# Kernel optimization log

Hardware: AMD Instinct MI355X
Metric: run time of the kernel (lower is better)

The kernel has to match this reference:

```python
import jax, jax.numpy as jnp
import numpy as np

H = 128
NH = 8  # num attention heads


def _ln(x, g, b, eps=1e-5):
    m = x.mean(-1, keepdims=True)
    v = ((x - m) ** 2).mean(-1, keepdims=True)
    return (x - m) / jnp.sqrt(v + eps) * g + b


def _mha(q_in, kv_in, Wqkv, bqkv, Wo, bo):
    # torch nn.MultiheadAttention with packed in_proj, batch=1, eval (no dropout)
    h = q_in.shape[-1]
    hd = h // NH
    Wq, Wk, Wv = Wqkv[:h], Wqkv[h:2 * h], Wqkv[2 * h:]
    bq, bk, bv = bqkv[:h], bqkv[h:2 * h], bqkv[2 * h:]
    q = (q_in @ Wq.T + bq).reshape(-1, NH, hd).transpose(1, 0, 2)   # [nh, Nq, hd]
    k = (kv_in @ Wk.T + bk).reshape(-1, NH, hd).transpose(1, 0, 2)  # [nh, Nk, hd]
    v = (kv_in @ Wv.T + bv).reshape(-1, NH, hd).transpose(1, 0, 2)
    scores = jnp.einsum('hqd,hkd->hqk', q, k) / jnp.sqrt(jnp.asarray(hd, q.dtype))
    attn = jax.nn.softmax(scores, axis=-1)
    out = jnp.einsum('hqk,hkd->hqd', attn, v)                       # [nh, Nq, hd]
    out = out.transpose(1, 0, 2).reshape(-1, h)
    return out @ Wo.T + bo


def setup_inputs() -> dict:
    key = jax.random.key(0)
    ks = jax.random.split(key, 32)
    s = 0.05
    d = {
        'ligand_features': jax.random.normal(ks[0], (512, 128), jnp.float32),
        'pocket_features': jax.random.normal(ks[1], (1024, 128), jnp.float32),
        'ligand_coords': jax.random.uniform(ks[2], (512, 3), jnp.float32) * 20.0,
        'pocket_coords': jax.random.uniform(ks[3], (1024, 3), jnp.float32) * 20.0,
        # projections
        'Wl': jax.random.normal(ks[4], (H, 128), jnp.float32) * s,
        'bl': jnp.zeros((H,), jnp.float32),
        'Wp': jax.random.normal(ks[5], (H, 128), jnp.float32) * s,
        'bp': jnp.zeros((H,), jnp.float32),
        # distance encoder: 1 -> h/4 -> h/2 -> h
        'Wd1': jax.random.normal(ks[6], (H // 4, 1), jnp.float32) * s,
        'bd1': jnp.zeros((H // 4,), jnp.float32),
        'Wd2': jax.random.normal(ks[7], (H // 2, H // 4), jnp.float32) * s,
        'bd2': jnp.zeros((H // 2,), jnp.float32),
        'Wd3': jax.random.normal(ks[8], (H, H // 2), jnp.float32) * s,
        'bd3': jnp.zeros((H,), jnp.float32),
        # gates
        'Wgl': jax.random.normal(ks[9], (H, 2 * H), jnp.float32) * s,
        'bgl': jnp.zeros((H,), jnp.float32),
        'Wgp': jax.random.normal(ks[10], (H, 2 * H), jnp.float32) * s,
        'bgp': jnp.zeros((H,), jnp.float32),
        # shared cross-attention (packed qkv like torch)
        'Wqkv': jax.random.normal(ks[11], (3 * H, H), jnp.float32) * s,
        'bqkv': jnp.zeros((3 * H,), jnp.float32),
        'Wo': jax.random.normal(ks[12], (H, H), jnp.float32) * s,
        'bo': jnp.zeros((H,), jnp.float32),
        # layer norms
        'g_l': jnp.ones((H,), jnp.float32),
        'be_l': jnp.zeros((H,), jnp.float32),
        'g_p': jnp.ones((H,), jnp.float32),
        'be_p': jnp.zeros((H,), jnp.float32),
    }
    return d


def reference(ligand_features, pocket_features, ligand_coords, pocket_coords,
              Wl, bl, Wp, bp, Wd1, bd1, Wd2, bd2, Wd3, bd3,
              Wgl, bgl, Wgp, bgp, Wqkv, bqkv, Wo, bo,
              g_l, be_l, g_p, be_p):
    lig = ligand_features @ Wl.T + bl   # [Nl, H]
    poc = pocket_features @ Wp.T + bp   # [Np, H]

    # pairwise distances [Nl, Np]
    diff = ligand_coords[:, None, :] - pocket_coords[None, :, :]
    dist = jnp.sqrt(jnp.sum(diff * diff, axis=-1))

    # distance encoder MLP applied elementwise -> [Nl, Np, H]
    e = jax.nn.relu(dist[..., None] @ Wd1.T + bd1)
    e = jax.nn.relu(e @ Wd2.T + bd2)
    enc = e @ Wd3.T + bd3
    m = enc.mean(axis=-1)               # [Nl, Np]

    # ligand enhancement: softmax over pocket axis
    sw_l = jax.nn.softmax(-m, axis=-1)          # [Nl, Np]
    agg_l = sw_l @ poc                          # [Nl, H]
    gate_l = jax.nn.sigmoid(jnp.concatenate([lig, agg_l], axis=-1) @ Wgl.T + bgl)
    lig_enh = gate_l * lig + (1.0 - gate_l) * agg_l

    # pocket enhancement: transposed encoding, softmax over ligand axis
    sw_p = jax.nn.softmax(-m.T, axis=-1)        # [Np, Nl]
    agg_p = sw_p @ lig                          # [Np, H]
    gate_p = jax.nn.sigmoid(jnp.concatenate([poc, agg_p], axis=-1) @ Wgp.T + bgp)
    poc_enh = gate_p * poc + (1.0 - gate_p) * agg_p

    lig_att = _mha(lig_enh, poc_enh, Wqkv, bqkv, Wo, bo)
    poc_att = _mha(poc_enh, lig_enh, Wqkv, bqkv, Wo, bo)

    lig_fused = _ln(lig_enh + lig_att, g_l, be_l)
    poc_fused = _ln(poc_enh + poc_att, g_p, be_p)
    return (lig_fused, poc_fused)
```

## Files before the change

kernel.cpp:

```cpp
#include <hip/hip_runtime.h>
#include <math.h>

#define NL 512
#define NP 1024
#define HDIM 128

#define TAB_N 8192
#define DMAX 34.65f

#define M_OFF    128
#define WLT_OFF  (M_OFF)
#define WPT_OFF  (M_OFF + 16384)
#define WQT_OFF  (M_OFF + 32768)
#define WOT_OFF  (M_OFF + 81920)
#define WGLT_OFF (M_OFF + 98304)
#define WGPT_OFF (M_OFF + 131072)
#define LIG_OFF  (M_OFF + NL*NP)
#define POC_OFF  (LIG_OFF + NL*HDIM)
#define LENH_OFF (POC_OFF + NP*HDIM)
#define PENH_OFF (LENH_OFF + NL*HDIM)
#define QKVL_OFF (PENH_OFF + NP*HDIM)
#define QKVP_OFF (QKVL_OFF + NL*384)
#define PARTL_OFF (QKVP_OFF + NP*384)
#define PARTP_OFF (PARTL_OFF + 512*8*8*18)
#define TAB_OFF  QKVL_OFF

__device__ __forceinline__ float dot4f(float4 a, float4 b){
  return fmaf(a.x,b.x, fmaf(a.y,b.y, fmaf(a.z,b.z, a.w*b.w)));
}

__device__ __forceinline__ void tpose(const float* __restrict__ src, float* __restrict__ dst,
                                      int O, int K, int blk0, int t){
  int e0 = blk0*1024 + t*4;
  #pragma unroll
  for (int i = 0; i < 4; i++){
    int e = e0 + i;
    int o = e / K, k = e - o*K;
    dst[(size_t)k*O + o] = src[(size_t)o*K + k];
  }
}
__global__ __launch_bounds__(256) void transpose_all(const float* __restrict__ Wl, const float* __restrict__ Wp,
                                                     const float* __restrict__ Wqkv, const float* __restrict__ Wo,
                                                     const float* __restrict__ Wgl, const float* __restrict__ Wgp,
                                                     float* __restrict__ ws){
  int b = blockIdx.x, t = threadIdx.x;
  if      (b < 16)  tpose(Wl,   ws + WLT_OFF,  128, 128, b,       t);
  else if (b < 32)  tpose(Wp,   ws + WPT_OFF,  128, 128, b - 16,  t);
  else if (b < 80)  tpose(Wqkv, ws + WQT_OFF,  384, 128, b - 32,  t);
  else if (b < 96)  tpose(Wo,   ws + WOT_OFF,  128, 128, b - 80,  t);
  else if (b < 128) tpose(Wgl,  ws + WGLT_OFF, 128, 256, b - 96,  t);
  else              tpose(Wgp,  ws + WGPT_OFF, 128, 256, b - 128, t);
}

__global__ __launch_bounds__(256) void table_kernel(const float* __restrict__ Wd1, const float* __restrict__ bd1,
                                                    const float* __restrict__ Wd2, const float* __restrict__ bd2,
                                                    const float* __restrict__ Wd3, const float* __restrict__ bd3,
                                                    float* __restrict__ tab){
  __shared__ float sWd1[32], sbd1[32], sWd2[2048], sbd2[64], swd3m[64];
  __shared__ float sbd3m;
  int t = threadIdx.x;
  int idx = blockIdx.x * 256 + t;
  if (t < 64){
    float s = 0.f;
    #pragma unroll 8
    for (int i = 0; i < 128; i++) s += Wd3[i*64 + t];
    swd3m[t] = s * (1.f/128.f);
  } else if (t == 64){
    float s = 0.f;
    for (int i = 0; i < 128; i++) s += bd3[i];
    sbd3m = s * (1.f/128.f);
  } else if (t >= 128 && t < 160){ sWd1[t-128] = Wd1[t-128]; sbd1[t-128] = bd1[t-128]; }
  else if (t >= 160 && t < 224){ sbd2[t-160] = bd2[t-160]; }
  for (int k = t; k < 2048; k += 256) sWd2[k] = Wd2[k];
  __syncthreads();

  float d = (float)idx * (DMAX / (float)(TAB_N - 1));

  float4 e1q[8];
  const float4* w1q = (const float4*)sWd1;
  const float4* b1q = (const float4*)sbd1;
  #pragma unroll
  for (int k4 = 0; k4 < 8; k4++){
    float4 w = w1q[k4], b = b1q[k4];
    float4 e;
    e.x = fmaxf(fmaf(d, w.x, b.x), 0.f);
    e.y = fmaxf(fmaf(d, w.y, b.y), 0.f);
    e.z = fmaxf(fmaf(d, w.z, b.z), 0.f);
    e.w = fmaxf(fmaf(d, w.w, b.w), 0.f);
    e1q[k4] = e;
  }
  float mv = sbd3m;
  #pragma unroll 4
  for (int j2 = 0; j2 < 64; j2++){
    const float4* wrow = (const float4*)(sWd2 + j2*32);
    float a0 = 0.f, a1 = 0.f, a2 = 0.f, a3 = 0.f;
    #pragma unroll
    for (int k4 = 0; k4 < 8; k4++){
      float4 w = wrow[k4], e = e1q[k4];
      a0 = fmaf(w.x, e.x, a0);
      a1 = fmaf(w.y, e.y, a1);
      a2 = fmaf(w.z, e.z, a2);
      a3 = fmaf(w.w, e.w, a3);
    }
    float e2v = fmaxf(sbd2[j2] + ((a0+a1)+(a2+a3)), 0.f);
    mv = fmaf(swd3m[j2], e2v, mv);
  }
  tab[idx] = mv;
}

__global__ __launch_bounds__(1024) void proj_kernel(const float* __restrict__ lf, const float* __restrict__ pf,
                                                    const float* __restrict__ WlT, const float* __restrict__ bl,
                                                    const float* __restrict__ WpT, const float* __restrict__ bp,
                                                    float* __restrict__ lig, float* __restrict__ poc){
  int b = blockIdx.x, t = threadIdx.x;
  bool isLig = (b < 64);
  int r0 = isLig ? b*8 : (b - 64)*8;
  const float* in = (isLig ? lf : pf) + (size_t)r0*HDIM;
  const float* WT = isLig ? WlT : WpT;
  const float* bias = isLig ? bl : bp;
  float* out = (isLig ? lig : poc) + (size_t)r0*HDIM;
  __shared__ float sx[8*HDIM];
  sx[t] = in[t];
  __syncthreads();
  int r = t >> 7, col = t & 127;
  const float* xr = sx + r*HDIM;
  float acc = bias[col];
  #pragma unroll 8
  for (int k = 0; k < 128; k++) acc = fmaf(WT[k*128 + col], xr[k], acc);
  out[r*HDIM + col] = acc;
}

__global__ __launch_bounds__(1024) void agg_gate_fused(const float* __restrict__ lc, const float* __restrict__ pc,
                                                       const float* __restrict__ tab,
                                                       const float* __restrict__ lig, const float* __restrict__ poc,
                                                       const float* __restrict__ WglT, const float* __restrict__ bgl,
                                                       const float* __restrict__ WgpT, const float* __restrict__ bgp,
                                                       float* __restrict__ lenh, float* __restrict__ penh){
  int b = blockIdx.x, t = threadIdx.x;
  bool isLig = (b < NL/4);
  int r0 = isLig ? b*4 : (b - NL/4)*4;
  int n = isLig ? NP : NL;
  const float* myFeat = isLig ? lig : poc;
  const float* otherFeat = isLig ? poc : lig;
  const float* myC = isLig ? lc : pc;
  const float* otC = isLig ? pc : lc;

  __shared__ float w[4*NP];
  __shared__ float sx[4*HDIM];
  __shared__ float sa[4*HDIM];
  __shared__ float part[16*512];
  __shared__ float redm[16];
  __shared__ float sgm[4], sinv[4];

  int rr = t >> 8, u = t & 255;
  int lane = t & 63, wv = t >> 6;
  int row = r0 + rr;

  if (t < 512) sx[t] = myFeat[(size_t)r0*HDIM + t];

  float cx = myC[row*3+0], cy = myC[row*3+1], cz = myC[row*3+2];
  const float inv_h = (float)(TAB_N - 1) / DMAX;
  int per = n >> 8;

  float xs[4];
  float lmax = -1e30f;
  for (int k = 0; k < per; k++){
    int j = u + (k << 8);
    float ox = otC[j*3+0], oy = otC[j*3+1], oz = otC[j*3+2];
    float dx = cx-ox, dy = cy-oy, dz = cz-oz;
    float d = sqrtf(fmaf(dx,dx, fmaf(dy,dy, dz*dz)));
    float xf = d * inv_h;
    int i0 = (int)xf;
    i0 = (i0 > TAB_N-2) ? (TAB_N-2) : i0;
    float f = xf - (float)i0;
    float v0 = tab[i0], v1 = tab[i0+1];
    xs[k] = -fmaf(f, v1 - v0, v0);
    lmax = fmaxf(lmax, xs[k]);
  }
  float v = lmax;
  #pragma unroll
  for (int off = 32; off; off >>= 1) v = fmaxf(v, __shfl_down(v, off));
  if (lane == 0) redm[wv] = v;
  __syncthreads();
  if (t < 4) sgm[t] = fmaxf(fmaxf(redm[t*4+0], redm[t*4+1]), fmaxf(redm[t*4+2], redm[t*4+3]));
  __syncthreads();
  float gm = sgm[rr];
  float lsum = 0.f;
  for (int k = 0; k < per; k++){
    float e = __expf(xs[k] - gm);
    w[rr*NP + u + (k << 8)] = e;
    lsum += e;
  }
  v = lsum;
  #pragma unroll
  for (int off = 32; off; off >>= 1) v += __shfl_down(v, off);
  if (lane == 0) redm[wv] = v;
  __syncthreads();
  if (t < 4) sinv[t] = 1.0f / ((redm[t*4+0] + redm[t*4+1]) + (redm[t*4+2] + redm[t*4+3]));
  __syncthreads();

  {
    int jg = t >> 6;
    int rp = (t >> 5) & 1;
    int c4 = t & 31;
    int per2 = n >> 4;
    int jb0 = jg * per2;
    int rA = rp*2, rB = rp*2 + 1;
    const float4* of4 = (const float4*)otherFeat;
    const float* wA = w + rA*NP;
    const float* wB = w + rB*NP;
    float4 accA = {0,0,0,0}, accB = {0,0,0,0};
    #pragma unroll 4
    for (int jj = 0; jj < per2; jj++){
      int j = jb0 + jj;
      float4 f = of4[(size_t)j*32 + c4];
      float w0 = wA[j], w1 = wB[j];
      accA.x = fmaf(w0, f.x, accA.x); accA.y = fmaf(w0, f.y, accA.y);
      accA.z = fmaf(w0, f.z, accA.z); accA.w = fmaf(w0, f.w, accA.w);
      accB.x = fmaf(w1, f.x, accB.x); accB.y = fmaf(w1, f.y, accB.y);
      accB.z = fmaf(w1, f.z, accB.z); accB.w = fmaf(w1, f.w, accB.w);
    }
    float4* p4 = (float4*)part;
    p4[jg*128 + rA*32 + c4] = accA;
    p4[jg*128 + rB*32 + c4] = accB;
  }
  __syncthreads();
  {
    float4* p4 = (float4*)part;
    #pragma unroll
    for (int s = 8; s >= 1; s >>= 1){
      if (t < s*128){
        int jg2 = t >> 7, rem = t & 127;
        float4 a = p4[jg2*128 + rem], bb = p4[(jg2+s)*128 + rem];
        a.x += bb.x; a.y += bb.y; a.z += bb.z; a.w += bb.w;
        p4[jg2*128 + rem] = a;
      }
      __syncthreads();
    }
  }
  if (t < 512){
    int r = t >> 7;
    sa[t] = part[t] * sinv[r];
  }
  __syncthreads();

  if (t < 512){
    int r = t >> 7, col = t & 127;
    const float* WT = isLig ? WglT : WgpT;
    const float* bg = isLig ? bgl : bgp;
    const float* xr = sx + r*HDIM;
    const float* ar = sa + r*HDIM;
    float g = bg[col];
    #pragma unroll 8
    for (int k = 0; k < 128; k++) g = fmaf(WT[k*128 + col], xr[k], g);
    #pragma unroll 8
    for (int k = 0; k < 128; k++) g = fmaf(WT[(128+k)*128 + col], ar[k], g);
    g = 1.0f / (1.0f + __expf(-g));
    float xv = xr[col], av = ar[col];
    float* dst = isLig ? (lenh + (size_t)(r0+r)*HDIM) : (penh + (size_t)(r0+r)*HDIM);
    dst[col] = fmaf(g, xv - av, av);
  }
}

__global__ __launch_bounds__(768) void qkv_kernel(const float* __restrict__ lenh, const float* __restrict__ penh,
                                                  const float* __restrict__ WqkvT, const float* __restrict__ bqkv,
                                                  float* __restrict__ qkvl, float* __restrict__ qkvp){
  int b = blockIdx.x, t = threadIdx.x;
  int row0 = b*2;
  bool isLig = (row0 < NL);
  int rloc = isLig ? row0 : row0 - NL;
  const float* in = (isLig ? lenh : penh) + (size_t)rloc*HDIM;
  float* out = (isLig ? qkvl : qkvp) + (size_t)rloc*384;
  __shared__ float sx[2*HDIM];
  if (t < 256) sx[t] = in[t];
  __syncthreads();
  int r = (t >= 384) ? 1 : 0;
  int col = t - r*384;
  const float* xr = sx + r*HDIM;
  float acc = bqkv[col];
  #pragma unroll 8
  for (int k = 0; k < 128; k++) acc = fmaf(WqkvT[k*384 + col], xr[k], acc);
  out[r*384 + col] = acc;
}

__global__ __launch_bounds__(256) void attn_part(const float* __restrict__ qkvl, const float* __restrict__ qkvp,
                                                 float* __restrict__ partL, float* __restrict__ partP){
  int bx = blockIdx.x;
  int t = threadIdx.x;
  const float* qsrc; const float* kvsrc; int qt, slice; bool isLig;
  if (bx < 256){ isLig = true;  qt = bx >> 3; slice = bx & 7; qsrc = qkvl; kvsrc = qkvp; }
  else { int b2 = bx - 256; isLig = false; qt = b2 >> 2; slice = b2 & 3; qsrc = qkvp; kvsrc = qkvl; }
  int g = t >> 7, tt = t & 127;
  int h = tt >> 4, q = tt & 15;
  int j0 = slice*128 + g*64;

  const float4* qp = (const float4*)(qsrc + (size_t)(qt*16+q)*384 + h*16);
  float4 q0 = qp[0], q1 = qp[1], q2 = qp[2], q3 = qp[3];
  float m = -1e30f, l = 0.f;
  float4 O0 = {0,0,0,0}, O1 = {0,0,0,0}, O2 = {0,0,0,0}, O3 = {0,0,0,0};

  __shared__ float sKV[8192];
  float* myKV = sKV + g*4096;

  for (int tile = 0; tile < 4; tile++){
    int jbase = j0 + tile*16;
    __syncthreads();
    #pragma unroll
    for (int n = 0; n < 8; n++){
      int v4 = tt + n*128;
      int jj = v4 >> 6, c4 = v4 & 63;
      ((float4*)myKV)[(size_t)jj*64 + c4] = *(const float4*)(kvsrc + (size_t)(jbase+jj)*384 + 128 + c4*4);
    }
    __syncthreads();
    float s[16];
    #pragma unroll
    for (int jj = 0; jj < 16; jj++){
      const float4* kk = (const float4*)(myKV + jj*256 + h*16);
      s[jj] = (dot4f(q0, kk[0]) + dot4f(q1, kk[1]) + dot4f(q2, kk[2]) + dot4f(q3, kk[3])) * 0.25f;
    }
    float mt = s[0];
    #pragma unroll
    for (int jj = 1; jj < 16; jj++) mt = fmaxf(mt, s[jj]);
    float mn = fmaxf(m, mt);
    float corr = __expf(m - mn);
    l *= corr;
    O0.x*=corr; O0.y*=corr; O0.z*=corr; O0.w*=corr;
    O1.x*=corr; O1.y*=corr; O1.z*=corr; O1.w*=corr;
    O2.x*=corr; O2.y*=corr; O2.z*=corr; O2.w*=corr;
    O3.x*=corr; O3.y*=corr; O3.z*=corr; O3.w*=corr;
    #pragma unroll
    for (int jj = 0; jj < 16; jj++){
      float p = __expf(s[jj] - mn);
      l += p;
      const float4* vv = (const float4*)(myKV + jj*256 + 128 + h*16);
      O0.x = fmaf(p, vv[0].x, O0.x); O0.y = fmaf(p, vv[0].y, O0.y);
      O0.z = fmaf(p, vv[0].z, O0.z); O0.w = fmaf(p, vv[0].w, O0.w);
      O1.x = fmaf(p, vv[1].x, O1.x); O1.y = fmaf(p, vv[1].y, O1.y);
      O1.z = fmaf(p, vv[1].z, O1.z); O1.w = fmaf(p, vv[1].w, O1.w);
      O2.x = fmaf(p, vv[2].x, O2.x); O2.y = fmaf(p, vv[2].y, O2.y);
      O2.z = fmaf(p, vv[2].z, O2.z); O2.w = fmaf(p, vv[2].w, O2.w);
      O3.x = fmaf(p, vv[3].x, O3.x); O3.y = fmaf(p, vv[3].y, O3.y);
      O3.z = fmaf(p, vv[3].z, O3.z); O3.w = fmaf(p, vv[3].w, O3.w);
    }
    m = mn;
  }

  __syncthreads();
  float* smerge = sKV;
  if (g == 1){
    float* b = smerge + tt*19;
    b[0] = m; b[1] = l;
    b[2]=O0.x; b[3]=O0.y; b[4]=O0.z; b[5]=O0.w;
    b[6]=O1.x; b[7]=O1.y; b[8]=O1.z; b[9]=O1.w;
    b[10]=O2.x; b[11]=O2.y; b[12]=O2.z; b[13]=O2.w;
    b[14]=O3.x; b[15]=O3.y; b[16]=O3.z; b[17]=O3.w;
  }
  __syncthreads();
  if (g == 0){
    const float* b = smerge + tt*19;
    float m1 = b[0], l1 = b[1];
    float M = fmaxf(m, m1);
    float e0 = __expf(m - M), e1 = __expf(m1 - M);
    float L = l*e0 + l1*e1;
    float* dst;
    if (isLig) dst = partL + ((size_t)((qt*16+q)*8 + h)*8 + slice)*18;
    else       dst = partP + ((size_t)((qt*16+q)*8 + h)*4 + slice)*18;
    dst[0] = M; dst[1] = L;
    dst[2]  = O0.x*e0 + b[2]*e1;  dst[3]  = O0.y*e0 + b[3]*e1;
    dst[4]  = O0.z*e0 + b[4]*e1;  dst[5]  = O0.w*e0 + b[5]*e1;
    dst[6]  = O1.x*e0 + b[6]*e1;  dst[7]  = O1.y*e0 + b[7]*e1;
    dst[8]  = O1.z*e0 + b[8]*e1;  dst[9]  = O1.w*e0 + b[9]*e1;
    dst[10] = O2.x*e0 + b[10]*e1; dst[11] = O2.y*e0 + b[11]*e1;
    dst[12] = O2.z*e0 + b[12]*e1; dst[13] = O2.w*e0 + b[13]*e1;
    dst[14] = O3.x*e0 + b[14]*e1; dst[15] = O3.y*e0 + b[15]*e1;
    dst[16] = O3.z*e0 + b[16]*e1; dst[17] = O3.w*e0 + b[17]*e1;
  }
}

__global__ __launch_bounds__(1024) void merge_ln(const float* __restrict__ partL, const float* __restrict__ partP,
                                                 const float* __restrict__ lenh, const float* __restrict__ penh,
                                                 const float* __restrict__ WoT, const float* __restrict__ bo,
                                                 const float* __restrict__ g_l, const float* __restrict__ be_l,
                                                 const float* __restrict__ g_p, const float* __restrict__ be_p,
                                                 float* __restrict__ out){
  int b = blockIdx.x, t = threadIdx.x;
  int r0 = b*8;
  int r = t >> 7, c = t & 127;
  int gr = r0 + r;
  int h = c >> 4, cc = c & 15;
  int ns; const float* base;
  if (gr < NL){ ns = 8; base = partL + ((size_t)(gr*8 + h))*8*18; }
  else        { ns = 4; base = partP + ((size_t)((gr-NL)*8 + h))*4*18; }
  float M = -1e30f;
  for (int s = 0; s < ns; s++) M = fmaxf(M, base[s*18]);
  float Lsum = 0.f, Osum = 0.f;
  for (int s = 0; s < ns; s++){
    float e = __expf(base[s*18] - M);
    Lsum = fmaf(e, base[s*18+1], Lsum);
    Osum = fmaf(e, base[s*18+2+cc], Osum);
  }
  __shared__ float sAtt[8*HDIM];
  sAtt[t] = Osum / Lsum;
  __syncthreads();
  float o = bo[c];
  const float* sA = sAtt + r*HDIM;
  #pragma unroll 8
  for (int k = 0; k < 128; k++) o = fmaf(WoT[k*128 + c], sA[k], o);
  const float* enh = (gr < NL) ? (lenh + (size_t)gr*HDIM) : (penh + (size_t)(gr-NL)*HDIM);
  float x = enh[c] + o;
  __shared__ float sred[32];
  int wid = t >> 6;
  float v = x;
  #pragma unroll
  for (int off = 32; off; off >>= 1) v += __shfl_down(v, off);
  if ((t & 63) == 0) sred[wid] = v;
  __syncthreads();
  float mu = (sred[2*r] + sred[2*r+1]) * (1.f/128.f);
  float dx = x - mu;
  v = dx*dx;
  #pragma unroll
  for (int off = 32; off; off >>= 1) v += __shfl_down(v, off);
  if ((t & 63) == 0) sred[16 + wid] = v;
  __syncthreads();
  float var = (sred[16 + 2*r] + sred[16 + 2*r+1]) * (1.f/128.f);
  float y = dx * rsqrtf(var + 1e-5f);
  if (gr < NL) y = fmaf(y, g_l[c], be_l[c]);
  else         y = fmaf(y, g_p[c], be_p[c]);
  out[(size_t)gr*HDIM + c] = y;
}

extern "C" void kernel_launch(void* const* d_in, const int* in_sizes, int n_in,
                              void* d_out, int out_size, void* d_ws, size_t ws_size,
                              hipStream_t stream){
  const float* lf   = (const float*)d_in[0];
  const float* pf   = (const float*)d_in[1];
  const float* lc   = (const float*)d_in[2];
  const float* pc   = (const float*)d_in[3];
  const float* Wl   = (const float*)d_in[4];
  const float* bl   = (const float*)d_in[5];
  const float* Wp   = (const float*)d_in[6];
  const float* bp   = (const float*)d_in[7];
  const float* Wd1  = (const float*)d_in[8];
  const float* bd1  = (const float*)d_in[9];
  const float* Wd2  = (const float*)d_in[10];
  const float* bd2  = (const float*)d_in[11];
  const float* Wd3  = (const float*)d_in[12];
  const float* bd3  = (const float*)d_in[13];
  const float* Wgl  = (const float*)d_in[14];
  const float* bgl  = (const float*)d_in[15];
  const float* Wgp  = (const float*)d_in[16];
  const float* bgp  = (const float*)d_in[17];
  const float* Wqkv = (const float*)d_in[18];
  const float* bqkv = (const float*)d_in[19];
  const float* Wo   = (const float*)d_in[20];
  const float* bo   = (const float*)d_in[21];
  const float* g_l  = (const float*)d_in[22];
  const float* be_l = (const float*)d_in[23];
  const float* g_p  = (const float*)d_in[24];
  const float* be_p = (const float*)d_in[25];

  float* ws  = (float*)d_ws;
  float* out = (float*)d_out;
  float* lig   = ws + LIG_OFF;
  float* poc   = ws + POC_OFF;
  float* lenh  = ws + LENH_OFF;
  float* penh  = ws + PENH_OFF;
  float* qkvl  = ws + QKVL_OFF;
  float* qkvp  = ws + QKVP_OFF;
  float* partL = ws + PARTL_OFF;
  float* partP = ws + PARTP_OFF;
  float* tab   = ws + TAB_OFF;

  transpose_all<<<160, 256, 0, stream>>>(Wl, Wp, Wqkv, Wo, Wgl, Wgp, ws);
  table_kernel<<<TAB_N/256, 256, 0, stream>>>(Wd1, bd1, Wd2, bd2, Wd3, bd3, tab);
  proj_kernel<<<192, 1024, 0, stream>>>(lf, pf, ws + WLT_OFF, bl, ws + WPT_OFF, bp, lig, poc);
  agg_gate_fused<<<NL/4 + NP/4, 1024, 0, stream>>>(lc, pc, tab, lig, poc,
                                                   ws + WGLT_OFF, bgl, ws + WGPT_OFF, bgp, lenh, penh);
  qkv_kernel<<<768, 768, 0, stream>>>(lenh, penh, ws + WQT_OFF, bqkv, qkvl, qkvp);
  attn_part<<<512, 256, 0, stream>>>(qkvl, qkvp, partL, partP);
  merge_ln<<<192, 1024, 0, stream>>>(partL, partP, lenh, penh, ws + WOT_OFF, bo,
                                     g_l, be_l, g_p, be_p, out);
}
```

Measured before the change: 209.4 us.

## Fuse prep kernels, fold QKV projection into gate kernel, restructure attention partials

Merges the weight-transpose and distance-table kernels into a single launch, with the table moved to its own workspace slot so it no longer aliases the QKV buffer. The QKV projection is computed inside the aggregation/gate kernel from the enhanced rows still in shared memory, which removes one launch and one global round trip of the enhanced features. The attention partial kernel now has each thread handle two query rows over 4 key groups of 32 instead of 2 groups of 64, so K/V values loaded from shared memory are reused across queries, followed by a 4-way merge. The fused QKV step runs on only 512 of 1024 threads per block, and the attention change raises register pressure.

```diff
diff --git a/kernel.cpp b/kernel.cpp
--- a/kernel.cpp
+++ b/kernel.cpp
@@ -15,6 +15,7 @@
 #define WOT_OFF  (M_OFF + 81920)
 #define WGLT_OFF (M_OFF + 98304)
 #define WGPT_OFF (M_OFF + 131072)
+#define TAB_OFF  (M_OFF + 163840)
 #define LIG_OFF  (M_OFF + NL*NP)
 #define POC_OFF  (LIG_OFF + NL*HDIM)
 #define LENH_OFF (POC_OFF + NP*HDIM)
@@ -23,7 +24,6 @@
 #define QKVP_OFF (QKVL_OFF + NL*384)
 #define PARTL_OFF (QKVP_OFF + NP*384)
 #define PARTP_OFF (PARTL_OFF + 512*8*8*18)
-#define TAB_OFF  QKVL_OFF
 
 __device__ __forceinline__ float dot4f(float4 a, float4 b){
   return fmaf(a.x,b.x, fmaf(a.y,b.y, fmaf(a.z,b.z, a.w*b.w)));
@@ -39,27 +39,27 @@
     dst[(size_t)k*O + o] = src[(size_t)o*K + k];
   }
 }
-__global__ __launch_bounds__(256) void transpose_all(const float* __restrict__ Wl, const float* __restrict__ Wp,
-                                                     const float* __restrict__ Wqkv, const float* __restrict__ Wo,
-                                                     const float* __restrict__ Wgl, const float* __restrict__ Wgp,
-                                                     float* __restrict__ ws){
+__global__ __launch_bounds__(256) void prep_all(const float* __restrict__ Wl, const float* __restrict__ Wp,
+                                                const float* __restrict__ Wqkv, const float* __restrict__ Wo,
+                                                const float* __restrict__ Wgl, const float* __restrict__ Wgp,
+                                                const float* __restrict__ Wd1, const float* __restrict__ bd1,
+                                                const float* __restrict__ Wd2, const float* __restrict__ bd2,
+                                                const float* __restrict__ Wd3, const float* __restrict__ bd3,
+                                                float* __restrict__ ws){
   int b = blockIdx.x, t = threadIdx.x;
-  if      (b < 16)  tpose(Wl,   ws + WLT_OFF,  128, 128, b,       t);
-  else if (b < 32)  tpose(Wp,   ws + WPT_OFF,  128, 128, b - 16,  t);
-  else if (b < 80)  tpose(Wqkv, ws + WQT_OFF,  384, 128, b - 32,  t);
-  else if (b < 96)  tpose(Wo,   ws + WOT_OFF,  128, 128, b - 80,  t);
-  else if (b < 128) tpose(Wgl,  ws + WGLT_OFF, 128, 256, b - 96,  t);
-  else              tpose(Wgp,  ws + WGPT_OFF, 128, 256, b - 128, t);
-}
-
-__global__ __launch_bounds__(256) void table_kernel(const float* __restrict__ Wd1, const float* __restrict__ bd1,
-                                                    const float* __restrict__ Wd2, const float* __restrict__ bd2,
-                                                    const float* __restrict__ Wd3, const float* __restrict__ bd3,
-                                                    float* __restrict__ tab){
+  if (b < 160){
+    if      (b < 16)  tpose(Wl,   ws + WLT_OFF,  128, 128, b,       t);
+    else if (b < 32)  tpose(Wp,   ws + WPT_OFF,  128, 128, b - 16,  t);
+    else if (b < 80)  tpose(Wqkv, ws + WQT_OFF,  384, 128, b - 32,  t);
+    else if (b < 96)  tpose(Wo,   ws + WOT_OFF,  128, 128, b - 80,  t);
+    else if (b < 128) tpose(Wgl,  ws + WGLT_OFF, 128, 256, b - 96,  t);
+    else              tpose(Wgp,  ws + WGPT_OFF, 128, 256, b - 128, t);
+    return;
+  }
+  float* tab = ws + TAB_OFF;
   __shared__ float sWd1[32], sbd1[32], sWd2[2048], sbd2[64], swd3m[64];
   __shared__ float sbd3m;
-  int t = threadIdx.x;
-  int idx = blockIdx.x * 256 + t;
+  int idx = (b - 160) * 256 + t;
   if (t < 64){
     float s = 0.f;
     #pragma unroll 8
@@ -75,18 +75,17 @@
   __syncthreads();
 
   float d = (float)idx * (DMAX / (float)(TAB_N - 1));
-
   float4 e1q[8];
   const float4* w1q = (const float4*)sWd1;
   const float4* b1q = (const float4*)sbd1;
   #pragma unroll
   for (int k4 = 0; k4 < 8; k4++){
-    float4 w = w1q[k4], b = b1q[k4];
+    float4 w = w1q[k4], bb = b1q[k4];
     float4 e;
-    e.x = fmaxf(fmaf(d, w.x, b.x), 0.f);
-    e.y = fmaxf(fmaf(d, w.y, b.y), 0.f);
-    e.z = fmaxf(fmaf(d, w.z, b.z), 0.f);
-    e.w = fmaxf(fmaf(d, w.w, b.w), 0.f);
+    e.x = fmaxf(fmaf(d, w.x, bb.x), 0.f);
+    e.y = fmaxf(fmaf(d, w.y, bb.y), 0.f);
+    e.z = fmaxf(fmaf(d, w.z, bb.z), 0.f);
+    e.w = fmaxf(fmaf(d, w.w, bb.w), 0.f);
     e1q[k4] = e;
   }
   float mv = sbd3m;
@@ -135,7 +134,9 @@
                                                        const float* __restrict__ lig, const float* __restrict__ poc,
                                                        const float* __restrict__ WglT, const float* __restrict__ bgl,
                                                        const float* __restrict__ WgpT, const float* __restrict__ bgp,
-                                                       float* __restrict__ lenh, float* __restrict__ penh){
+                                                       const float* __restrict__ WqkvT, const float* __restrict__ bqkv,
+                                                       float* __restrict__ lenh, float* __restrict__ penh,
+                                                       float* __restrict__ qkvl, float* __restrict__ qkvp){
   int b = blockIdx.x, t = threadIdx.x;
   bool isLig = (b < NL/4);
   int r0 = isLig ? b*4 : (b - NL/4)*4;
@@ -244,43 +245,45 @@
   }
   __syncthreads();
 
+  float enh_val = 0.f;
+  {
+    if (t < 512){
+      int r = t >> 7, col = t & 127;
+      const float* WT = isLig ? WglT : WgpT;
+      const float* bg = isLig ? bgl : bgp;
+      const float* xr = sx + r*HDIM;
+      const float* ar = sa + r*HDIM;
+      float g = bg[col];
+      #pragma unroll 8
+      for (int k = 0; k < 128; k++) g = fmaf(WT[k*128 + col], xr[k], g);
+      #pragma unroll 8
+      for (int k = 0; k < 128; k++) g = fmaf(WT[(128+k)*128 + col], ar[k], g);
+      g = 1.0f / (1.0f + __expf(-g));
+      float xv = xr[col], av = ar[col];
+      enh_val = fmaf(g, xv - av, av);
+      float* dst = isLig ? (lenh + (size_t)(r0+r)*HDIM) : (penh + (size_t)(r0+r)*HDIM);
+      dst[col] = enh_val;
+    }
+  }
+  __syncthreads();
+  if (t < 512) sa[t] = enh_val;
+  __syncthreads();
+
   if (t < 512){
-    int r = t >> 7, col = t & 127;
-    const float* WT = isLig ? WglT : WgpT;
-    const float* bg = isLig ? bgl : bgp;
-    const float* xr = sx + r*HDIM;
-    const float* ar = sa + r*HDIM;
-    float g = bg[col];
-    #pragma unroll 8
-    for (int k = 0; k < 128; k++) g = fmaf(WT[k*128 + col], xr[k], g);
-    #pragma unroll 8
-    for (int k = 0; k < 128; k++) g = fmaf(WT[(128+k)*128 + col], ar[k], g);
-    g = 1.0f / (1.0f + __expf(-g));
-    float xv = xr[col], av = ar[col];
-    float* dst = isLig ? (lenh + (size_t)(r0+r)*HDIM) : (penh + (size_t)(r0+r)*HDIM);
-    dst[col] = fmaf(g, xv - av, av);
-  }
-}
-
-__global__ __launch_bounds__(768) void qkv_kernel(const float* __restrict__ lenh, const float* __restrict__ penh,
-                                                  const float* __restrict__ WqkvT, const float* __restrict__ bqkv,
-                                                  float* __restrict__ qkvl, float* __restrict__ qkvp){
-  int b = blockIdx.x, t = threadIdx.x;
-  int row0 = b*2;
-  bool isLig = (row0 < NL);
-  int rloc = isLig ? row0 : row0 - NL;
-  const float* in = (isLig ? lenh : penh) + (size_t)rloc*HDIM;
-  float* out = (isLig ? qkvl : qkvp) + (size_t)rloc*384;
-  __shared__ float sx[2*HDIM];
-  if (t < 256) sx[t] = in[t];
-  __syncthreads();
-  int r = (t >= 384) ? 1 : 0;
-  int col = t - r*384;
-  const float* xr = sx + r*HDIM;
-  float acc = bqkv[col];
-  #pragma unroll 8
-  for (int k = 0; k < 128; k++) acc = fmaf(WqkvT[k*384 + col], xr[k], acc);
-  out[r*384 + col] = acc;
+    int r = t >> 7, c0 = t & 127;
+    const float* er = sa + r*HDIM;
+    float acc0 = bqkv[c0], acc1 = bqkv[c0+128], acc2 = bqkv[c0+256];
+    #pragma unroll 4
+    for (int k = 0; k < 128; k++){
+      float xv = er[k];
+      const float* wk = WqkvT + k*384;
+      acc0 = fmaf(wk[c0],       xv, acc0);
+      acc1 = fmaf(wk[c0+128],   xv, acc1);
+      acc2 = fmaf(wk[c0+256],   xv, acc2);
+    }
+    float* qout = (isLig ? qkvl : qkvp) + (size_t)(r0+r)*384;
+    qout[c0] = acc0; qout[c0+128] = acc1; qout[c0+256] = acc2;
+  }
 }
 
 __global__ __launch_bounds__(256) void attn_part(const float* __restrict__ qkvl, const float* __restrict__ qkvp,
@@ -290,90 +293,137 @@
   const float* qsrc; const float* kvsrc; int qt, slice; bool isLig;
   if (bx < 256){ isLig = true;  qt = bx >> 3; slice = bx & 7; qsrc = qkvl; kvsrc = qkvp; }
   else { int b2 = bx - 256; isLig = false; qt = b2 >> 2; slice = b2 & 3; qsrc = qkvp; kvsrc = qkvl; }
-  int g = t >> 7, tt = t & 127;
-  int h = tt >> 4, q = tt & 15;
-  int j0 = slice*128 + g*64;
-
-  const float4* qp = (const float4*)(qsrc + (size_t)(qt*16+q)*384 + h*16);
-  float4 q0 = qp[0], q1 = qp[1], q2 = qp[2], q3 = qp[3];
-  float m = -1e30f, l = 0.f;
-  float4 O0 = {0,0,0,0}, O1 = {0,0,0,0}, O2 = {0,0,0,0}, O3 = {0,0,0,0};
+  int g = t >> 6, tt = t & 63;
+  int h = tt >> 3, qp = tt & 7;
+  int j0 = slice*128 + g*32;
+
+  const float4* qA = (const float4*)(qsrc + (size_t)(qt*16+qp)*384 + h*16);
+  const float4* qB = (const float4*)(qsrc + (size_t)(qt*16+qp+8)*384 + h*16);
+  float4 a0 = qA[0], a1 = qA[1], a2 = qA[2], a3 = qA[3];
+  float4 b0 = qB[0], b1 = qB[1], b2 = qB[2], b3 = qB[3];
+  float mA = -1e30f, lA = 0.f, mB = -1e30f, lB = 0.f;
+  float4 OA0={0,0,0,0}, OA1={0,0,0,0}, OA2={0,0,0,0}, OA3={0,0,0,0};
+  float4 OB0={0,0,0,0}, OB1={0,0,0,0}, OB2={0,0,0,0}, OB3={0,0,0,0};
 
   __shared__ float sKV[8192];
-  float* myKV = sKV + g*4096;
+  float* myKV = sKV + g*2048;
 
   for (int tile = 0; tile < 4; tile++){
-    int jbase = j0 + tile*16;
+    int jbase = j0 + tile*8;
     __syncthreads();
     #pragma unroll
-    for (int n = 0; n < 8; n++){
-      int v4 = tt + n*128;
+    for (int nn = 0; nn < 8; nn++){
+      int v4 = tt + nn*64;
       int jj = v4 >> 6, c4 = v4 & 63;
-      ((float4*)myKV)[(size_t)jj*64 + c4] = *(const float4*)(kvsrc + (size_t)(jbase+jj)*384 + 128 + c4*4);
+      ((float4*)myKV)[jj*64 + c4] = *(const float4*)(kvsrc + (size_t)(jbase+jj)*384 + 128 + c4*4);
     }
     __syncthreads();
-    float s[16];
-    #pragma unroll
-    for (int jj = 0; jj < 16; jj++){
+    float sA[8], sB[8];
+    #pragma unroll
+    for (int jj = 0; jj < 8; jj++){
       const float4* kk = (const float4*)(myKV + jj*256 + h*16);
-      s[jj] = (dot4f(q0, kk[0]) + dot4f(q1, kk[1]) + dot4f(q2, kk[2]) + dot4f(q3, kk[3])) * 0.25f;
-    }
-    float mt = s[0];
-    #pragma unroll
-    for (int jj = 1; jj < 16; jj++) mt = fmaxf(mt, s[jj]);
-    float mn = fmaxf(m, mt);
-    float corr = __expf(m - mn);
-    l *= corr;
-    O0.x*=corr; O0.y*=corr; O0.z*=corr; O0.w*=corr;
-    O1.x*=corr; O1.y*=corr; O1.z*=corr; O1.w*=corr;
-    O2.x*=corr; O2.y*=corr; O2.z*=corr; O2.w*=corr;
-    O3.x*=corr; O3.y*=corr; O3.z*=corr; O3.w*=corr;
-    #pragma unroll
-    for (int jj = 0; jj < 16; jj++){
-      float p = __expf(s[jj] - mn);
-      l += p;
+      float4 k0 = kk[0], k1 = kk[1], k2 = kk[2], k3 = kk[3];
+      sA[jj] = (dot4f(a0,k0) + dot4f(a1,k1) + dot4f(a2,k2) + dot4f(a3,k3)) * 0.25f;
+      sB[jj] = (dot4f(b0,k0) + dot4f(b1,k1) + dot4f(b2,k2) + dot4f(b3,k3)) * 0.25f;
+    }
+    float mtA = sA[0], mtB = sB[0];
+    #pragma unroll
+    for (int jj = 1; jj < 8; jj++){ mtA = fmaxf(mtA, sA[jj]); mtB = fmaxf(mtB, sB[jj]); }
+    float mnA = fmaxf(mA, mtA), mnB = fmaxf(mB, mtB);
+    float cA = __expf(mA - mnA), cB = __expf(mB - mnB);
+    lA *= cA; lB *= cB;
+    OA0.x*=cA; OA0.y*=cA; OA0.z*=cA; OA0.w*=cA;
+    OA1.x*=cA; OA1.y*=cA; OA1.z*=cA; OA1.w*=cA;
+    OA2.x*=cA; OA2.y*=cA; OA2.z*=cA; OA2.w*=cA;
+    OA3.x*=cA; OA3.y*=cA; OA3.z*=cA; OA3.w*=cA;
+    OB0.x*=cB; OB0.y*=cB; OB0.z*=cB; OB0.w*=cB;
+    OB1.x*=cB; OB1.y*=cB; OB1.z*=cB; OB1.w*=cB;
+    OB2.x*=cB; OB2.y*=cB; OB2.z*=cB; OB2.w*=cB;
+    OB3.x*=cB; OB3.y*=cB; OB3.z*=cB; OB3.w*=cB;
+    #pragma unroll
+    for (int jj = 0; jj < 8; jj++){
+      float pA = __expf(sA[jj] - mnA);
+      float pB = __expf(sB[jj] - mnB);
+      lA += pA; lB += pB;
       const float4* vv = (const float4*)(myKV + jj*256 + 128 + h*16);
-      O0.x = fmaf(p, vv[0].x, O0.x); O0.y = fmaf(p, vv[0].y, O0.y);
-      O0.z = fmaf(p, vv[0].z, O0.z); O0.w = fmaf(p, vv[0].w, O0.w);
-      O1.x = fmaf(p, vv[1].x, O1.x); O1.y = fmaf(p, vv[1].y, O1.y);
-      O1.z = fmaf(p, vv[1].z, O1.z); O1.w = fmaf(p, vv[1].w, O1.w);
-      O2.x = fmaf(p, vv[2].x, O2.x); O2.y = fmaf(p, vv[2].y, O2.y);
-      O2.z = fmaf(p, vv[2].z, O2.z); O2.w = fmaf(p, vv[2].w, O2.w);
-      O3.x = fmaf(p, vv[3].x, O3.x); O3.y = fmaf(p, vv[3].y, O3.y);
-      O3.z = fmaf(p, vv[3].z, O3.z); O3.w = fmaf(p, vv[3].w, O3.w);
-    }
-    m = mn;
-  }
-
-  __syncthreads();
-  float* smerge = sKV;
-  if (g == 1){
-    float* b = smerge + tt*19;
-    b[0] = m; b[1] = l;
-    b[2]=O0.x; b[3]=O0.y; b[4]=O0.z; b[5]=O0.w;
-    b[6]=O1.x; b[7]=O1.y; b[8]=O1.z; b[9]=O1.w;
-    b[10]=O2.x; b[11]=O2.y; b[12]=O2.z; b[13]=O2.w;
-    b[14]=O3.x; b[15]=O3.y; b[16]=O3.z; b[17]=O3.w;
+      float4 v0 = vv[0], v1 = vv[1], v2 = vv[2], v3 = vv[3];
+      OA0.x = fmaf(pA, v0.x, OA0.x); OA0.y = fmaf(pA, v0.y, OA0.y);
+      OA0.z = fmaf(pA, v0.z, OA0.z); OA0.w = fmaf(pA, v0.w, OA0.w);
+      OA1.x = fmaf(pA, v1.x, OA1.x); OA1.y = fmaf(pA, v1.y, OA1.y);
+      OA1.z = fmaf(pA, v1.z, OA1.z); OA1.w = fmaf(pA, v1.w, OA1.w);
+      OA2.x = fmaf(pA, v2.x, OA2.x); OA2.y = fmaf(pA, v2.y, OA2.y);
+      OA2.z = fmaf(pA, v2.z, OA2.z); OA2.w = fmaf(pA, v2.w, OA2.w);
+      OA3.x = fmaf(pA, v3.x, OA3.x); OA3.y = fmaf(pA, v3.y, OA3.y);
+      OA3.z = fmaf(pA, v3.z, OA3.z); OA3.w = fmaf(pA, v3.w, OA3.w);
+      OB0.x = fmaf(pB, v0.x, OB0.x); OB0.y = fmaf(pB, v0.y, OB0.y);
+      OB0.z = fmaf(pB, v0.z, OB0.z); OB0.w = fmaf(pB, v0.w, OB0.w);
+      OB1.x = fmaf(pB, v1.x, OB1.x); OB1.y = fmaf(pB, v1.y, OB1.y);
+      OB1.z = fmaf(pB, v1.z, OB1.z); OB1.w = fmaf(pB, v1.w, OB1.w);
+      OB2.x = fmaf(pB, v2.x, OB2.x); OB2.y = fmaf(pB, v2.y, OB2.y);
+      OB2.z = fmaf(pB, v2.z, OB2.z); OB2.w = fmaf(pB, v2.w, OB2.w);
+      OB3.x = fmaf(pB, v3.x, OB3.x); OB3.y = fmaf(pB, v3.y, OB3.y);
+      OB3.z = fmaf(pB, v3.z, OB3.z); OB3.w = fmaf(pB, v3.w, OB3.w);
+    }
+    mA = mnA; mB = mnB;
+  }
+
+  __syncthreads();
+  if (g > 0){
+    float* bA = sKV + (size_t)((g-1)*128 + tt*2)*19;
+    bA[0]=mA; bA[1]=lA;
+    bA[2]=OA0.x; bA[3]=OA0.y; bA[4]=OA0.z; bA[5]=OA0.w;
+    bA[6]=OA1.x; bA[7]=OA1.y; bA[8]=OA1.z; bA[9]=OA1.w;
+    bA[10]=OA2.x; bA[11]=OA2.y; bA[12]=OA2.z; bA[13]=OA2.w;
+    bA[14]=OA3.x; bA[15]=OA3.y; bA[16]=OA3.z; bA[17]=OA3.w;
+    float* bB = bA + 19;
+    bB[0]=mB; bB[1]=lB;
+    bB[2]=OB0.x; bB[3]=OB0.y; bB[4]=OB0.z; bB[5]=OB0.w;
+    bB[6]=OB1.x; bB[7]=OB1.y; bB[8]=OB1.z; bB[9]=OB1.w;
+    bB[10]=OB2.x; bB[11]=OB2.y; bB[12]=OB2.z; bB[13]=OB2.w;
+    bB[14]=OB3.x; bB[15]=OB3.y; bB[16]=OB3.z; bB[17]=OB3.w;
   }
   __syncthreads();
   if (g == 0){
-    const float* b = smerge + tt*19;
-    float m1 = b[0], l1 = b[1];
-    float M = fmaxf(m, m1);
-    float e0 = __expf(m - M), e1 = __expf(m1 - M);
-    float L = l*e0 + l1*e1;
-    float* dst;
-    if (isLig) dst = partL + ((size_t)((qt*16+q)*8 + h)*8 + slice)*18;
-    else       dst = partP + ((size_t)((qt*16+q)*8 + h)*4 + slice)*18;
+    float M = mA, L = lA;
+    float O[16] = {OA0.x,OA0.y,OA0.z,OA0.w, OA1.x,OA1.y,OA1.z,OA1.w,
+                   OA2.x,OA2.y,OA2.z,OA2.w, OA3.x,OA3.y,OA3.z,OA3.w};
+    #pragma unroll
+    for (int gg = 1; gg < 4; gg++){
+      const float* br = sKV + (size_t)((gg-1)*128 + tt*2)*19;
+      float m1 = br[0], l1 = br[1];
+      float Mn = fmaxf(M, m1);
+      float e0 = __expf(M - Mn), e1 = __expf(m1 - Mn);
+      L = L*e0 + l1*e1;
+      #pragma unroll
+      for (int k = 0; k < 16; k++) O[k] = O[k]*e0 + br[2+k]*e1;
+      M = Mn;
+    }
+    int rowA = qt*16 + qp;
+    float* dst = isLig ? (partL + ((size_t)(rowA*8 + h)*8 + slice)*18)
+                       : (partP + ((size_t)(rowA*8 + h)*4 + slice)*18);
     dst[0] = M; dst[1] = L;
-    dst[2]  = O0.x*e0 + b[2]*e1;  dst[3]  = O0.y*e0 + b[3]*e1;
-    dst[4]  = O0.z*e0 + b[4]*e1;  dst[5]  = O0.w*e0 + b[5]*e1;
-    dst[6]  = O1.x*e0 + b[6]*e1;  dst[7]  = O1.y*e0 + b[7]*e1;
-    dst[8]  = O1.z*e0 + b[8]*e1;  dst[9]  = O1.w*e0 + b[9]*e1;
-    dst[10] = O2.x*e0 + b[10]*e1; dst[11] = O2.y*e0 + b[11]*e1;
-    dst[12] = O2.z*e0 + b[12]*e1; dst[13] = O2.w*e0 + b[13]*e1;
-    dst[14] = O3.x*e0 + b[14]*e1; dst[15] = O3.y*e0 + b[15]*e1;
-    dst[16] = O3.z*e0 + b[16]*e1; dst[17] = O3.w*e0 + b[17]*e1;
+    #pragma unroll
+    for (int k = 0; k < 16; k++) dst[2+k] = O[k];
+    M = mB; L = lB;
+    float Ob[16] = {OB0.x,OB0.y,OB0.z,OB0.w, OB1.x,OB1.y,OB1.z,OB1.w,
+                    OB2.x,OB2.y,OB2.z,OB2.w, OB3.x,OB3.y,OB3.z,OB3.w};
+    #pragma unroll
+    for (int gg = 1; gg < 4; gg++){
+      const float* br = sKV + (size_t)((gg-1)*128 + tt*2 + 1)*19;
+      float m1 = br[0], l1 = br[1];
+      float Mn = fmaxf(M, m1);
+      float e0 = __expf(M - Mn), e1 = __expf(m1 - Mn);
+      L = L*e0 + l1*e1;
+      #pragma unroll
+      for (int k = 0; k < 16; k++) Ob[k] = Ob[k]*e0 + br[2+k]*e1;
+      M = Mn;
+    }
+    int rowB = qt*16 + qp + 8;
+    float* dstB = isLig ? (partL + ((size_t)(rowB*8 + h)*8 + slice)*18)
+                        : (partP + ((size_t)(rowB*8 + h)*4 + slice)*18);
+    dstB[0] = M; dstB[1] = L;
+    #pragma unroll
+    for (int k = 0; k < 16; k++) dstB[2+k] = Ob[k];
   }
 }
 
@@ -471,12 +521,12 @@
   float* partP = ws + PARTP_OFF;
   float* tab   = ws + TAB_OFF;
 
-  transpose_all<<<160, 256, 0, stream>>>(Wl, Wp, Wqkv, Wo, Wgl, Wgp, ws);
-  table_kernel<<<TAB_N/256, 256, 0, stream>>>(Wd1, bd1, Wd2, bd2, Wd3, bd3, tab);
+  prep_all<<<192, 256, 0, stream>>>(Wl, Wp, Wqkv, Wo, Wgl, Wgp, Wd1, bd1, Wd2, bd2, Wd3, bd3, ws);
   proj_kernel<<<192, 1024, 0, stream>>>(lf, pf, ws + WLT_OFF, bl, ws + WPT_OFF, bp, lig, poc);
   agg_gate_fused<<<NL/4 + NP/4, 1024, 0, stream>>>(lc, pc, tab, lig, poc,
-                                                   ws + WGLT_OFF, bgl, ws + WGPT_OFF, bgp, lenh, penh);
-  qkv_kernel<<<768, 768, 0, stream>>>(lenh, penh, ws + WQT_OFF, bqkv, qkvl, qkvp);
+                                                   ws + WGLT_OFF, bgl, ws + WGPT_OFF, bgp,
+                                                   ws + WQT_OFF, bqkv,
+                                                   lenh, penh, qkvl, qkvp);
   attn_part<<<512, 256, 0, stream>>>(qkvl, qkvp, partL, partP);
   merge_ln<<<192, 1024, 0, stream>>>(partL, partP, lenh, penh, ws + WOT_OFF, bo,
                                      g_l, be_l, g_p, be_p, out);
```

Result: faster. 198.1 us (-5.4%).
